# Kernel tuning notes

Hardware: AMD Instinct MI355X
Metric: run time of the kernel (lower is better)

Reference implementation:

```python
import jax, jax.numpy as jnp
import numpy as np

IN_F, OUT_F, RANK, ALPHA, NUM_ADAPTERS = 1024, 1024, 8, 1.0, 8
B, S = 32, 1024
SCALE = ALPHA / RANK


def setup_inputs() -> dict:
    key = jax.random.key(0)
    k1, k2, k3, k4, k5, k6 = jax.random.split(key, 6)
    x = jax.random.normal(k1, (B, S, IN_F), dtype=jnp.float32)
    subject_id = jax.random.randint(k2, (B,), 0, NUM_ADAPTERS)
    # base linear: W [out,in], bias [out] (torch nn.Linear layout)
    W = jax.random.normal(k3, (OUT_F, IN_F), dtype=jnp.float32) * (1.0 / np.sqrt(IN_F))
    b = jax.random.normal(k4, (OUT_F,), dtype=jnp.float32) * 0.01
    # stacked LoRA weights: A [E, rank, in], Bw [E, out, rank]
    # (original inits Bw to zeros; randomized here so the LoRA path is exercised)
    A = jax.random.normal(k5, (NUM_ADAPTERS, RANK, IN_F), dtype=jnp.float32) * 0.02
    Bw = jax.random.normal(k6, (NUM_ADAPTERS, OUT_F, RANK), dtype=jnp.float32) * 0.02
    return {"x": x, "W": W, "b": b, "A": A, "Bw": Bw, "subject_id": subject_id}


def reference(x, W, b, A, Bw, subject_id):
    # base linear: [B,S,O]
    out = jnp.einsum("bsd,od->bso", x, W) + b
    # gather per-batch adapter weights (equivalent to the per-adapter mask loop)
    A_sel = A[subject_id]   # [B, rank, in]
    B_sel = Bw[subject_id]  # [B, out, rank]
    h = jnp.einsum("bsd,brd->bsr", x, A_sel)          # [B,S,rank]
    lora = jnp.einsum("bsr,bor->bso", h, B_sel) * SCALE  # [B,S,out]
    return out + lora
```

## Files before the change

kernel.cpp:

```cpp
#include <hip/hip_runtime.h>
#include <hip/hip_bf16.h>

typedef __bf16 bf16_t;
typedef bf16_t bf16x4 __attribute__((ext_vector_type(4)));
typedef bf16_t bf16x8 __attribute__((ext_vector_type(8)));
typedef float  f32x4  __attribute__((ext_vector_type(4)));

#define IN_F   1024
#define OUT_F  1024
#define RANK   8
#define NE     8
#define BATCH  32
#define SEQ    1024
#define M_TOT  (BATCH * SEQ)
#define SCALE  0.125f
#define NT     16

#define GLOAD_LDS16(g, l)                                                     \
  __builtin_amdgcn_global_load_lds(                                           \
      (const __attribute__((address_space(1))) void*)(g),                     \
      (__attribute__((address_space(3))) void*)(l), 16, 0, 0)

#define CFENCE asm volatile("" ::: "memory")
#define BAR()                                                                 \
  do { CFENCE; __builtin_amdgcn_s_barrier(); CFENCE; } while (0)
#define VMCNT(n) asm volatile("s_waitcnt vmcnt(" #n ")" ::: "memory")

__global__ __launch_bounds__(256) void build_weff(
    const float* __restrict__ W, const float* __restrict__ A,
    const float* __restrict__ Bw, bf16_t* __restrict__ weff) {
  const int e  = blockIdx.x >> 10;
  const int o  = blockIdx.x & 1023;
  const int d0 = threadIdx.x << 2;

  f32x4 acc = *(const f32x4*)(W + ((size_t)o << 10) + d0);
  const float* bwr = Bw + (((size_t)e << 10) + o) * RANK;
  const float* ab  = A + (((size_t)e * RANK) << 10) + d0;
#pragma unroll
  for (int r = 0; r < RANK; ++r) {
    const float s = SCALE * bwr[r];
    const f32x4 a4 = *(const f32x4*)(ab + ((size_t)r << 10));
    acc += s * a4;
  }
  bf16x4 ov;
#pragma unroll
  for (int j = 0; j < 4; ++j) ov[j] = (bf16_t)acc[j];
  *(bf16x4*)(weff + (((size_t)e << 10) + o) * IN_F + d0) = ov;
}

__global__ __launch_bounds__(256) void cvt_x(const float* __restrict__ x,
                                             bf16_t* __restrict__ xb, int n4) {
  int i = blockIdx.x * 256 + threadIdx.x;
  const int stride = gridDim.x * 256;
  for (; i < n4; i += stride) {
    const f32x4 v = *(const f32x4*)(x + ((size_t)i << 2));
    bf16x4 o;
#pragma unroll
    for (int j = 0; j < 4; ++j) o[j] = (bf16_t)v[j];
    *(bf16x4*)(xb + ((size_t)i << 2)) = o;
  }
}

__global__ __launch_bounds__(512, 2) void gemm256(
    const bf16_t* __restrict__ xb, const bf16_t* __restrict__ weff,
    const float* __restrict__ bias, const int* __restrict__ sid,
    float* __restrict__ out) {
  __shared__ bf16_t lds[2][2][2][8192];

  const int bid0 = blockIdx.x;
  const int wgid = ((bid0 & 7) << 6) + (bid0 >> 3);
  const int mb = wgid >> 2, nb = wgid & 3;
  const int m0 = mb << 8, n0 = nb << 8;
  const int e = sid[mb >> 2];

  const int tid = threadIdx.x;
  const int lane = tid & 63, wid = tid >> 6;
  const int wm = wid >> 2, wn = wid & 3;

  const bf16_t* agbase = xb + ((size_t)m0 << 10);
  const bf16_t* bgbase = weff + ((size_t)e << 20) + ((size_t)n0 << 10);

  int soff[2];
#pragma unroll
  for (int i = 0; i < 2; ++i) {
    const int r = (wid << 5) + (i << 4) + (lane >> 2);
    const int sg = (lane & 3) ^ ((r >> 1) & 3);
    soff[i] = (r << 10) + (sg << 3);
  }

  int aoff[8], boff[4];
#pragma unroll
  for (int mi = 0; mi < 8; ++mi) {
    const int r = (wm << 7) + (mi << 4) + (lane & 15);
    const int g = (lane >> 4) ^ ((r >> 1) & 3);
    aoff[mi] = (r << 5) + (g << 3);
  }
#pragma unroll
  for (int ni = 0; ni < 4; ++ni) {
    const int r = (wn << 6) + (ni << 4) + (lane & 15);
    const int g = (lane >> 4) ^ ((r >> 1) & 3);
    boff[ni] = (r << 5) + (g << 3);
  }

  f32x4 acc[8][4] = {};

#define STAGE2(kt, kh)                                                        \
  do {                                                                        \
    bf16_t* _da = &lds[(kt) & 1][0][kh][wid << 10];                           \
    bf16_t* _db = &lds[(kt) & 1][1][kh][wid << 10];                           \
    const int _kc = ((kt) << 6) + ((kh) << 5);                                \
    GLOAD_LDS16(agbase + _kc + soff[0], _da);                                 \
    GLOAD_LDS16(agbase + _kc + soff[1], _da + 512);                           \
    GLOAD_LDS16(bgbase + _kc + soff[0], _db);                                 \
    GLOAD_LDS16(bgbase + _kc + soff[1], _db + 512);                           \
  } while (0)

#define PHASE_READS(kt, kh)                                                   \
  do {                                                                        \
    const bf16_t* _ab = &lds[(kt) & 1][0][kh][0];                             \
    const bf16_t* _bb = &lds[(kt) & 1][1][kh][0];                             \
    _Pragma("unroll") for (int mi = 0; mi < 8; ++mi)                          \
        af[mi] = *(const bf16x8*)(_ab + aoff[mi]);                            \
    _Pragma("unroll") for (int ni = 0; ni < 4; ++ni)                          \
        bfr[ni] = *(const bf16x8*)(_bb + boff[ni]);                           \
  } while (0)

#define MFMAS()                                                               \
  do {                                                                        \
    __builtin_amdgcn_s_setprio(1);                                            \
    _Pragma("unroll") for (int mi = 0; mi < 8; ++mi)                          \
        _Pragma("unroll") for (int ni = 0; ni < 4; ++ni)                      \
            acc[mi][ni] = __builtin_amdgcn_mfma_f32_16x16x32_bf16(            \
                af[mi], bfr[ni], acc[mi][ni], 0, 0, 0);                       \
    __builtin_amdgcn_s_setprio(0);                                            \
  } while (0)

  STAGE2(0, 0);
  STAGE2(0, 1);

  bf16x8 af[8], bfr[4];
  for (int j = 0; j < NT - 1; ++j) {
    VMCNT(4);
    BAR();
    PHASE_READS(j, 0);
    STAGE2(j + 1, 0);
    MFMAS();
    VMCNT(4);
    BAR();
    PHASE_READS(j, 1);
    STAGE2(j + 1, 1);
    MFMAS();
  }
  VMCNT(4);
  BAR();
  PHASE_READS(NT - 1, 0);
  MFMAS();
  VMCNT(0);
  BAR();
  PHASE_READS(NT - 1, 1);
  MFMAS();

  const int R0 = m0 + (wm << 7);
  const int C0 = n0 + (wn << 6);
  const int crow = (lane >> 4) << 2;
  const int ccol = lane & 15;
#pragma unroll
  for (int ni = 0; ni < 4; ++ni) {
    const int col = C0 + (ni << 4) + ccol;
    const float bv = bias[col];
#pragma unroll
    for (int mi = 0; mi < 8; ++mi) {
      const int row = R0 + (mi << 4) + crow;
#pragma unroll
      for (int j2 = 0; j2 < 4; ++j2)
        __builtin_nontemporal_store(acc[mi][ni][j2] + bv,
                                    &out[((size_t)(row + j2) << 10) + col]);
    }
  }
#undef STAGE2
#undef PHASE_READS
#undef MFMAS
}

__global__ __launch_bounds__(256) void lora_naive(
    const float* __restrict__ x, const float* __restrict__ W,
    const float* __restrict__ bias, const float* __restrict__ A,
    const float* __restrict__ Bw, const int* __restrict__ sid,
    float* __restrict__ out) {
  const int m = blockIdx.x;
  const int e = sid[m >> 10];
  __shared__ float xs[IN_F];
  __shared__ float h[RANK];
  const int tid = threadIdx.x;
  for (int i = tid; i < IN_F; i += 256) xs[i] = x[((size_t)m << 10) + i];
  __syncthreads();
  if (tid < RANK) {
    float s = 0.f;
    const float* ar = A + (((size_t)e * RANK + tid) << 10);
    for (int d = 0; d < IN_F; ++d) s += xs[d] * ar[d];
    h[tid] = s * SCALE;
  }
  __syncthreads();
  for (int o = tid; o < OUT_F; o += 256) {
    const float* wr = W + ((size_t)o << 10);
    float s = 0.f;
    for (int d = 0; d < IN_F; ++d) s += xs[d] * wr[d];
    const float* bwr = Bw + (((size_t)e << 10) + o) * RANK;
    float l = 0.f;
#pragma unroll
    for (int r = 0; r < RANK; ++r) l += h[r] * bwr[r];
    out[((size_t)m << 10) + o] = s + bias[o] + l;
  }
}

extern "C" void kernel_launch(void* const* d_in, const int* in_sizes, int n_in,
                              void* d_out, int out_size, void* d_ws,
                              size_t ws_size, hipStream_t stream) {
  const float* x   = (const float*)d_in[0];
  const float* W   = (const float*)d_in[1];
  const float* b   = (const float*)d_in[2];
  const float* A   = (const float*)d_in[3];
  const float* Bw  = (const float*)d_in[4];
  const int*   sid = (const int*)d_in[5];
  float* out = (float*)d_out;

  const size_t weff_bytes = (size_t)NE * OUT_F * IN_F * 2;
  const size_t xb_bytes   = (size_t)M_TOT * IN_F * 2;

  if (ws_size >= weff_bytes + xb_bytes) {
    bf16_t* weff = (bf16_t*)d_ws;
    bf16_t* xb   = (bf16_t*)((char*)d_ws + weff_bytes);
    hipLaunchKernelGGL(build_weff, dim3(NE * OUT_F), dim3(256), 0, stream,
                       W, A, Bw, weff);
    hipLaunchKernelGGL(cvt_x, dim3(4096), dim3(256), 0, stream,
                       x, xb, M_TOT * IN_F / 4);
    hipLaunchKernelGGL(gemm256, dim3((M_TOT / 256) * (OUT_F / 256)),
                       dim3(512), 0, stream, xb, weff, b, sid, out);
  } else {
    hipLaunchKernelGGL(lora_naive, dim3(M_TOT), dim3(256), 0, stream,
                       x, W, b, A, Bw, sid, out);
  }
}
```

Baseline: 128.3 us.

## Restructure GEMM pipeline with separate A/B LDS rings and B-fragment prefetch

Replaces the combined double-buffered A/B stage scheme with a 2-slot A ring and a 4-slot B ring. B is staged two k-steps ahead, and B fragments are read into registers one phase early using alternating register sets. Each phase now waits for all outstanding loads (vmcnt 0) before its barrier, where the old code allowed 4 loads in flight. The aim is to hide LDS read latency for B, at the cost of more registers, more LDS, and possibly less global-load overlap because of the full waits.

```diff
diff --git a/kernel.cpp b/kernel.cpp
--- a/kernel.cpp
+++ b/kernel.cpp
@@ -14,7 +14,6 @@
 #define SEQ    1024
 #define M_TOT  (BATCH * SEQ)
 #define SCALE  0.125f
-#define NT     16
 
 #define GLOAD_LDS16(g, l)                                                     \
   __builtin_amdgcn_global_load_lds(                                           \
@@ -65,7 +64,8 @@
     const bf16_t* __restrict__ xb, const bf16_t* __restrict__ weff,
     const float* __restrict__ bias, const int* __restrict__ sid,
     float* __restrict__ out) {
-  __shared__ bf16_t lds[2][2][2][8192];
+  __shared__ bf16_t lds_a[2][8192];
+  __shared__ bf16_t lds_b[4][8192];
 
   const int bid0 = blockIdx.x;
   const int wgid = ((bid0 & 7) << 6) + (bid0 >> 3);
@@ -103,62 +103,90 @@
   }
 
   f32x4 acc[8][4] = {};
-
-#define STAGE2(kt, kh)                                                        \
-  do {                                                                        \
-    bf16_t* _da = &lds[(kt) & 1][0][kh][wid << 10];                           \
-    bf16_t* _db = &lds[(kt) & 1][1][kh][wid << 10];                           \
-    const int _kc = ((kt) << 6) + ((kh) << 5);                                \
-    GLOAD_LDS16(agbase + _kc + soff[0], _da);                                 \
-    GLOAD_LDS16(agbase + _kc + soff[1], _da + 512);                           \
-    GLOAD_LDS16(bgbase + _kc + soff[0], _db);                                 \
-    GLOAD_LDS16(bgbase + _kc + soff[1], _db + 512);                           \
-  } while (0)
-
-#define PHASE_READS(kt, kh)                                                   \
-  do {                                                                        \
-    const bf16_t* _ab = &lds[(kt) & 1][0][kh][0];                             \
-    const bf16_t* _bb = &lds[(kt) & 1][1][kh][0];                             \
+  bf16x8 af[8], bfrE[4], bfrO[4];
+
+#define ASTAGE(kp, ra)                                                        \
+  do {                                                                        \
+    bf16_t* _d = &lds_a[ra][wid << 10];                                       \
+    const int _kc = (kp) << 5;                                                \
+    GLOAD_LDS16(agbase + _kc + soff[0], _d);                                  \
+    GLOAD_LDS16(agbase + _kc + soff[1], _d + 512);                            \
+  } while (0)
+
+#define BSTAGE(kp, rb)                                                        \
+  do {                                                                        \
+    bf16_t* _d = &lds_b[rb][wid << 10];                                       \
+    const int _kc = (kp) << 5;                                                \
+    GLOAD_LDS16(bgbase + _kc + soff[0], _d);                                  \
+    GLOAD_LDS16(bgbase + _kc + soff[1], _d + 512);                            \
+  } while (0)
+
+#define READ_AF(ra)                                                           \
+  do {                                                                        \
+    const bf16_t* _ab = &lds_a[ra][0];                                        \
     _Pragma("unroll") for (int mi = 0; mi < 8; ++mi)                          \
         af[mi] = *(const bf16x8*)(_ab + aoff[mi]);                            \
+  } while (0)
+
+#define READ_BFR(SET, rb)                                                     \
+  do {                                                                        \
+    const bf16_t* _bb = &lds_b[rb][0];                                        \
     _Pragma("unroll") for (int ni = 0; ni < 4; ++ni)                          \
-        bfr[ni] = *(const bf16x8*)(_bb + boff[ni]);                           \
-  } while (0)
-
-#define MFMAS()                                                               \
+        SET[ni] = *(const bf16x8*)(_bb + boff[ni]);                           \
+  } while (0)
+
+#define MFMAS(SET)                                                            \
   do {                                                                        \
     __builtin_amdgcn_s_setprio(1);                                            \
     _Pragma("unroll") for (int mi = 0; mi < 8; ++mi)                          \
         _Pragma("unroll") for (int ni = 0; ni < 4; ++ni)                      \
             acc[mi][ni] = __builtin_amdgcn_mfma_f32_16x16x32_bf16(            \
-                af[mi], bfr[ni], acc[mi][ni], 0, 0, 0);                       \
+                af[mi], SET[ni], acc[mi][ni], 0, 0, 0);                       \
     __builtin_amdgcn_s_setprio(0);                                            \
   } while (0)
 
-  STAGE2(0, 0);
-  STAGE2(0, 1);
-
-  bf16x8 af[8], bfr[4];
-  for (int j = 0; j < NT - 1; ++j) {
-    VMCNT(4);
-    BAR();
-    PHASE_READS(j, 0);
-    STAGE2(j + 1, 0);
-    MFMAS();
-    VMCNT(4);
-    BAR();
-    PHASE_READS(j, 1);
-    STAGE2(j + 1, 1);
-    MFMAS();
-  }
-  VMCNT(4);
-  BAR();
-  PHASE_READS(NT - 1, 0);
-  MFMAS();
+  ASTAGE(0, 0);
+  BSTAGE(0, 0);
+  BSTAGE(1, 1);
   VMCNT(0);
   BAR();
-  PHASE_READS(NT - 1, 1);
-  MFMAS();
+  READ_BFR(bfrE, 0);
+
+  for (int jj = 0; jj < 7; ++jj) {
+    const int p = jj << 2;
+    VMCNT(0); BAR();
+    ASTAGE(p + 1, 1); BSTAGE(p + 2, 2);
+    READ_AF(0);  READ_BFR(bfrO, 1);
+    MFMAS(bfrE);
+    VMCNT(0); BAR();
+    ASTAGE(p + 2, 0); BSTAGE(p + 3, 3);
+    READ_AF(1);  READ_BFR(bfrE, 2);
+    MFMAS(bfrO);
+    VMCNT(0); BAR();
+    ASTAGE(p + 3, 1); BSTAGE(p + 4, 0);
+    READ_AF(0);  READ_BFR(bfrO, 3);
+    MFMAS(bfrE);
+    VMCNT(0); BAR();
+    ASTAGE(p + 4, 0); BSTAGE(p + 5, 1);
+    READ_AF(1);  READ_BFR(bfrE, 0);
+    MFMAS(bfrO);
+  }
+
+  VMCNT(0); BAR();
+  ASTAGE(29, 1); BSTAGE(30, 2);
+  READ_AF(0);  READ_BFR(bfrO, 1);
+  MFMAS(bfrE);
+  VMCNT(0); BAR();
+  ASTAGE(30, 0); BSTAGE(31, 3);
+  READ_AF(1);  READ_BFR(bfrE, 2);
+  MFMAS(bfrO);
+  VMCNT(0); BAR();
+  ASTAGE(31, 1);
+  READ_AF(0);  READ_BFR(bfrO, 3);
+  MFMAS(bfrE);
+  VMCNT(0); BAR();
+  READ_AF(1);
+  MFMAS(bfrO);
 
   const int R0 = m0 + (wm << 7);
   const int C0 = n0 + (wn << 6);
@@ -177,8 +205,10 @@
                                     &out[((size_t)(row + j2) << 10) + col]);
     }
   }
-#undef STAGE2
-#undef PHASE_READS
+#undef ASTAGE
+#undef BSTAGE
+#undef READ_AF
+#undef READ_BFR
 #undef MFMAS
 }
 
```

Result: slower. 145.9 us (+13.7%).

## Prepack merged LoRA weights into MFMA fragment order and load B directly to registers

Applied to the files above, without the earlier changes.

The weight-building kernel now writes the merged bf16 weights in MFMA fragment order, so the GEMM loads its B operand straight from global memory into registers with coalesced 16-byte loads instead of staging it through LDS. This halves LDS usage and LDS read traffic per tile. The pipeline is restructured so each 64-wide k-tile is processed whole, with one barrier and a full vmcnt(0) wait per tile, and register-prefetches the next B fragments. Output stores are switched from nontemporal to normal stores. The trade-off is higher register pressure from double-buffered B fragments and a full memory drain each tile, which can expose load latency.

```diff
diff --git a/kernel.cpp b/kernel.cpp
--- a/kernel.cpp
+++ b/kernel.cpp
@@ -26,26 +26,35 @@
   do { CFENCE; __builtin_amdgcn_s_barrier(); CFENCE; } while (0)
 #define VMCNT(n) asm volatile("s_waitcnt vmcnt(" #n ")" ::: "memory")
 
-__global__ __launch_bounds__(256) void build_weff(
+__global__ __launch_bounds__(256) void build_frag(
     const float* __restrict__ W, const float* __restrict__ A,
-    const float* __restrict__ Bw, bf16_t* __restrict__ weff) {
-  const int e  = blockIdx.x >> 10;
-  const int o  = blockIdx.x & 1023;
-  const int d0 = threadIdx.x << 2;
-
-  f32x4 acc = *(const f32x4*)(W + ((size_t)o << 10) + d0);
-  const float* bwr = Bw + (((size_t)e << 10) + o) * RANK;
-  const float* ab  = A + (((size_t)e * RANK) << 10) + d0;
+    const float* __restrict__ Bw, bf16_t* __restrict__ wfrag) {
+  const int wid = threadIdx.x >> 6, lane = threadIdx.x & 63;
+  const int L = (blockIdx.x << 2) + wid;
+  const int e  = L >> 11;
+  const int nb = (L >> 9) & 3;
+  const int kt = (L >> 5) & 15;
+  const int kh = (L >> 4) & 1;
+  const int wn = (L >> 2) & 3;
+  const int ni = L & 3;
+  const int o  = (nb << 8) + (wn << 6) + (ni << 4) + (lane & 15);
+  const int kb = (kt << 6) + (kh << 5) + ((lane >> 4) << 3);
+
+  const float* wrow = W + ((size_t)o << 10) + kb;
+  f32x4 s0 = *(const f32x4*)(wrow);
+  f32x4 s1 = *(const f32x4*)(wrow + 4);
+  const float* bwr = Bw + ((((size_t)e << 10) + o) << 3);
+  const float* ab  = A + (((size_t)e << 3) << 10) + kb;
 #pragma unroll
   for (int r = 0; r < RANK; ++r) {
-    const float s = SCALE * bwr[r];
-    const f32x4 a4 = *(const f32x4*)(ab + ((size_t)r << 10));
-    acc += s * a4;
-  }
-  bf16x4 ov;
-#pragma unroll
-  for (int j = 0; j < 4; ++j) ov[j] = (bf16_t)acc[j];
-  *(bf16x4*)(weff + (((size_t)e << 10) + o) * IN_F + d0) = ov;
+    const float c = SCALE * bwr[r];
+    s0 += c * *(const f32x4*)(ab + ((size_t)r << 10));
+    s1 += c * *(const f32x4*)(ab + ((size_t)r << 10) + 4);
+  }
+  bf16x8 v;
+#pragma unroll
+  for (int j = 0; j < 4; ++j) { v[j] = (bf16_t)s0[j]; v[4 + j] = (bf16_t)s1[j]; }
+  *(bf16x8*)(wfrag + ((size_t)L << 9) + (lane << 3)) = v;
 }
 
 __global__ __launch_bounds__(256) void cvt_x(const float* __restrict__ x,
@@ -62,15 +71,15 @@
 }
 
 __global__ __launch_bounds__(512, 2) void gemm256(
-    const bf16_t* __restrict__ xb, const bf16_t* __restrict__ weff,
+    const bf16_t* __restrict__ xb, const bf16_t* __restrict__ wfrag,
     const float* __restrict__ bias, const int* __restrict__ sid,
     float* __restrict__ out) {
-  __shared__ bf16_t lds[2][2][2][8192];
+  __shared__ bf16_t lds_a[2][2][8192];
 
   const int bid0 = blockIdx.x;
   const int wgid = ((bid0 & 7) << 6) + (bid0 >> 3);
   const int mb = wgid >> 2, nb = wgid & 3;
-  const int m0 = mb << 8, n0 = nb << 8;
+  const int m0 = mb << 8;
   const int e = sid[mb >> 2];
 
   const int tid = threadIdx.x;
@@ -78,7 +87,8 @@
   const int wm = wid >> 2, wn = wid & 3;
 
   const bf16_t* agbase = xb + ((size_t)m0 << 10);
-  const bf16_t* bgbase = weff + ((size_t)e << 20) + ((size_t)n0 << 10);
+  const bf16_t* bgf = wfrag + ((((size_t)e << 2) + nb) << 18) + (wn << 11) +
+                      (lane << 3);
 
   int soff[2];
 #pragma unroll
@@ -87,81 +97,79 @@
     const int sg = (lane & 3) ^ ((r >> 1) & 3);
     soff[i] = (r << 10) + (sg << 3);
   }
-
-  int aoff[8], boff[4];
+  int aoff[8];
 #pragma unroll
   for (int mi = 0; mi < 8; ++mi) {
     const int r = (wm << 7) + (mi << 4) + (lane & 15);
     const int g = (lane >> 4) ^ ((r >> 1) & 3);
     aoff[mi] = (r << 5) + (g << 3);
   }
-#pragma unroll
-  for (int ni = 0; ni < 4; ++ni) {
-    const int r = (wn << 6) + (ni << 4) + (lane & 15);
-    const int g = (lane >> 4) ^ ((r >> 1) & 3);
-    boff[ni] = (r << 5) + (g << 3);
-  }
 
   f32x4 acc[8][4] = {};
-
-#define STAGE2(kt, kh)                                                        \
-  do {                                                                        \
-    bf16_t* _da = &lds[(kt) & 1][0][kh][wid << 10];                           \
-    bf16_t* _db = &lds[(kt) & 1][1][kh][wid << 10];                           \
-    const int _kc = ((kt) << 6) + ((kh) << 5);                                \
-    GLOAD_LDS16(agbase + _kc + soff[0], _da);                                 \
-    GLOAD_LDS16(agbase + _kc + soff[1], _da + 512);                           \
-    GLOAD_LDS16(bgbase + _kc + soff[0], _db);                                 \
-    GLOAD_LDS16(bgbase + _kc + soff[1], _db + 512);                           \
-  } while (0)
-
-#define PHASE_READS(kt, kh)                                                   \
-  do {                                                                        \
-    const bf16_t* _ab = &lds[(kt) & 1][0][kh][0];                             \
-    const bf16_t* _bb = &lds[(kt) & 1][1][kh][0];                             \
+  bf16x8 af[8], bfr[2][2][4];
+
+#define ASTG(kt, c)                                                           \
+  do {                                                                        \
+    const int _k0 = (kt) << 6;                                                \
+    bf16_t* _d0 = &lds_a[c][0][wid << 10];                                    \
+    bf16_t* _d1 = &lds_a[c][1][wid << 10];                                    \
+    GLOAD_LDS16(agbase + _k0 + soff[0], _d0);                                 \
+    GLOAD_LDS16(agbase + _k0 + soff[1], _d0 + 512);                           \
+    GLOAD_LDS16(agbase + _k0 + 32 + soff[0], _d1);                            \
+    GLOAD_LDS16(agbase + _k0 + 32 + soff[1], _d1 + 512);                      \
+  } while (0)
+
+#define BLOAD(kt, S)                                                          \
+  do {                                                                        \
+    const bf16_t* _p = bgf + ((size_t)(kt) << 14);                            \
+    _Pragma("unroll") for (int _n = 0; _n < 4; ++_n)                          \
+        bfr[S][0][_n] = *(const bf16x8*)(_p + (_n << 9));                     \
+    _Pragma("unroll") for (int _n = 0; _n < 4; ++_n)                          \
+        bfr[S][1][_n] = *(const bf16x8*)(_p + 8192 + (_n << 9));              \
+  } while (0)
+
+#define RD(c, kh)                                                             \
+  do {                                                                        \
+    const bf16_t* _ab = &lds_a[c][kh][0];                                     \
     _Pragma("unroll") for (int mi = 0; mi < 8; ++mi)                          \
         af[mi] = *(const bf16x8*)(_ab + aoff[mi]);                            \
-    _Pragma("unroll") for (int ni = 0; ni < 4; ++ni)                          \
-        bfr[ni] = *(const bf16x8*)(_bb + boff[ni]);                           \
-  } while (0)
-
-#define MFMAS()                                                               \
+  } while (0)
+
+#define MM(S, kh)                                                             \
   do {                                                                        \
     __builtin_amdgcn_s_setprio(1);                                            \
     _Pragma("unroll") for (int mi = 0; mi < 8; ++mi)                          \
         _Pragma("unroll") for (int ni = 0; ni < 4; ++ni)                      \
             acc[mi][ni] = __builtin_amdgcn_mfma_f32_16x16x32_bf16(            \
-                af[mi], bfr[ni], acc[mi][ni], 0, 0, 0);                       \
+                af[mi], bfr[S][kh][ni], acc[mi][ni], 0, 0, 0);                \
     __builtin_amdgcn_s_setprio(0);                                            \
   } while (0)
 
-  STAGE2(0, 0);
-  STAGE2(0, 1);
-
-  bf16x8 af[8], bfr[4];
-  for (int j = 0; j < NT - 1; ++j) {
-    VMCNT(4);
-    BAR();
-    PHASE_READS(j, 0);
-    STAGE2(j + 1, 0);
-    MFMAS();
-    VMCNT(4);
-    BAR();
-    PHASE_READS(j, 1);
-    STAGE2(j + 1, 1);
-    MFMAS();
-  }
-  VMCNT(4);
-  BAR();
-  PHASE_READS(NT - 1, 0);
-  MFMAS();
+#define TILE(J, C, S, NXT, DO_ISSUE)                                          \
+  do {                                                                        \
+    RD(C, 0);                                                                 \
+    if (DO_ISSUE) { BLOAD((J) + 1, NXT); ASTG((J) + 1, 1 - (C)); }            \
+    MM(S, 0);                                                                 \
+    RD(C, 1);                                                                 \
+    MM(S, 1);                                                                 \
+    if (DO_ISSUE) { VMCNT(0); BAR(); }                                        \
+  } while (0)
+
+  BLOAD(0, 0);
+  ASTG(0, 0);
   VMCNT(0);
   BAR();
-  PHASE_READS(NT - 1, 1);
-  MFMAS();
+
+  for (int jj = 0; jj < 7; ++jj) {
+    const int j0 = jj << 1;
+    TILE(j0, 0, 0, 1, 1);
+    TILE(j0 + 1, 1, 1, 0, 1);
+  }
+  TILE(14, 0, 0, 1, 1);
+  TILE(15, 1, 1, 0, 0);
 
   const int R0 = m0 + (wm << 7);
-  const int C0 = n0 + (wn << 6);
+  const int C0 = (nb << 8) + (wn << 6);
   const int crow = (lane >> 4) << 2;
   const int ccol = lane & 15;
 #pragma unroll
@@ -173,13 +181,14 @@
       const int row = R0 + (mi << 4) + crow;
 #pragma unroll
       for (int j2 = 0; j2 < 4; ++j2)
-        __builtin_nontemporal_store(acc[mi][ni][j2] + bv,
-                                    &out[((size_t)(row + j2) << 10) + col]);
+        out[((size_t)(row + j2) << 10) + col] = acc[mi][ni][j2] + bv;
     }
   }
-#undef STAGE2
-#undef PHASE_READS
-#undef MFMAS
+#undef ASTG
+#undef BLOAD
+#undef RD
+#undef MM
+#undef TILE
 }
 
 __global__ __launch_bounds__(256) void lora_naive(
@@ -224,18 +233,18 @@
   const int*   sid = (const int*)d_in[5];
   float* out = (float*)d_out;
 
-  const size_t weff_bytes = (size_t)NE * OUT_F * IN_F * 2;
-  const size_t xb_bytes   = (size_t)M_TOT * IN_F * 2;
-
-  if (ws_size >= weff_bytes + xb_bytes) {
-    bf16_t* weff = (bf16_t*)d_ws;
-    bf16_t* xb   = (bf16_t*)((char*)d_ws + weff_bytes);
-    hipLaunchKernelGGL(build_weff, dim3(NE * OUT_F), dim3(256), 0, stream,
-                       W, A, Bw, weff);
+  const size_t wfrag_bytes = (size_t)NE * OUT_F * IN_F * 2;
+  const size_t xb_bytes    = (size_t)M_TOT * IN_F * 2;
+
+  if (ws_size >= wfrag_bytes + xb_bytes) {
+    bf16_t* wfrag = (bf16_t*)d_ws;
+    bf16_t* xb    = (bf16_t*)((char*)d_ws + wfrag_bytes);
+    hipLaunchKernelGGL(build_frag, dim3(4096), dim3(256), 0, stream,
+                       W, A, Bw, wfrag);
     hipLaunchKernelGGL(cvt_x, dim3(4096), dim3(256), 0, stream,
                        x, xb, M_TOT * IN_F / 4);
     hipLaunchKernelGGL(gemm256, dim3((M_TOT / 256) * (OUT_F / 256)),
-                       dim3(512), 0, stream, xb, weff, b, sid, out);
+                       dim3(512), 0, stream, xb, wfrag, b, sid, out);
   } else {
     hipLaunchKernelGGL(lora_naive, dim3(M_TOT), dim3(256), 0, stream,
                        x, W, b, A, Bw, sid, out);
```

Result: slower. 140.7 us (+9.7%).
